# Kernel optimization log

Measured on AMD Instinct MI355X. Metric: run time of the kernel, lower is better.

## Reference

```python
import jax, jax.numpy as jnp
import numpy as np

EPS = 1e-5

def layernorm(x, w, b):
    mu = jnp.mean(x, axis=-1, keepdims=True)
    var = jnp.mean((x - mu) ** 2, axis=-1, keepdims=True)
    return (x - mu) / jnp.sqrt(var + EPS) * w + b

def setup_inputs() -> dict:
    key = jax.random.key(0)
    ks = jax.random.split(key, 20)
    N, E, G = 50000, 800000, 512
    IN, OUT, TXT, MAN = 128, 128, 768, 14
    d = {
        "x": jax.random.normal(ks[0], (N, IN), jnp.float32),
        "edge_index": jax.random.randint(ks[1], (2, E), 0, N),
        "batch": jnp.sort(jax.random.randint(ks[2], (N,), 0, G)),
        "batch_size": G,
        "text_embedding": jax.random.normal(ks[3], (G, TXT), jnp.float32),
        "features_embedding": jax.random.normal(ks[4], (G, MAN), jnp.float32),
        # params
        "ln_proj_w": jnp.ones((IN,)), "ln_proj_b": jnp.zeros((IN,)),
        "W_l": jax.random.normal(ks[5], (IN, OUT)) / np.sqrt(IN),
        "b_l": jnp.zeros((OUT,)),
        "W_r": jax.random.normal(ks[6], (IN, OUT)) / np.sqrt(IN),
        "ln_conv_w": jnp.ones((OUT,)), "ln_conv_b": jnp.zeros((OUT,)),
        "gate_w": jax.random.normal(ks[7], (OUT, 1)) / np.sqrt(OUT),
        "gate_b": jnp.zeros((1,)),
        "graph_weight": jnp.asarray(1.0, jnp.float32),
        "msg_W": jax.random.normal(ks[8], (TXT, OUT)) / np.sqrt(TXT),
        "msg_b": jnp.zeros((OUT,)),
        "feat_W": jax.random.normal(ks[9], (MAN, OUT)) / np.sqrt(MAN),
        "feat_b": jnp.zeros((OUT,)),
        "mixed_w": jnp.ones((3 * OUT,)), "mixed_b": jnp.zeros((3 * OUT,)),
        "fc1_W": jax.random.normal(ks[10], (3 * OUT, 1)) / np.sqrt(3 * OUT),
        "fc1_b": jnp.zeros((1,)),
    }
    return d

def reference(x, edge_index, batch, batch_size, text_embedding, features_embedding,
              ln_proj_w, ln_proj_b, W_l, b_l, W_r, ln_conv_w, ln_conv_b,
              gate_w, gate_b, graph_weight, msg_W, msg_b, feat_W, feat_b,
              mixed_w, mixed_b, fc1_W, fc1_b):
    N = x.shape[0]
    src, dst = edge_index[0], edge_index[1]
    # project_norm
    h = layernorm(x, ln_proj_w, ln_proj_b)
    # GraphSAGE (SAGEConv, mean aggregation): out = mean_j(h_j) @ W_l + b + h @ W_r
    msgs = h[src]                                   # [E, IN] gather
    agg = jax.ops.segment_sum(msgs, dst, num_segments=N)
    deg = jax.ops.segment_sum(jnp.ones((src.shape[0],), h.dtype), dst, num_segments=N)
    mean_nb = agg / jnp.maximum(deg, 1.0)[:, None]
    h = mean_nb @ W_l + b_l + h @ W_r
    # layernorm + gelu (HomogeneousGraphConvolution)
    h = jax.nn.gelu(layernorm(h, ln_conv_w, ln_conv_b), approximate=False)
    # AttentionalAggregation: scatter-softmax over `batch`
    gate = (h @ gate_w + gate_b)[:, 0]              # [N]
    seg_max = jax.ops.segment_max(gate, batch, num_segments=batch_size)
    seg_max = jnp.where(jnp.isfinite(seg_max), seg_max, 0.0)
    e = jnp.exp(gate - seg_max[batch])
    denom = jax.ops.segment_sum(e, batch, num_segments=batch_size)
    attn = (e / denom[batch])[:, None]              # [N,1]
    graph_embedding = jax.ops.segment_sum(attn * h, batch, num_segments=batch_size)
    # dropout is identity in eval mode
    weighted = graph_weight * graph_embedding
    msg_emb = jax.nn.gelu(text_embedding @ msg_W + msg_b, approximate=False)
    feat_emb = jax.nn.gelu(features_embedding @ feat_W + feat_b, approximate=False)
    emb = jnp.concatenate([weighted, msg_emb, feat_emb], axis=1)
    emb = layernorm(emb, mixed_w, mixed_b)
    logits = emb @ fc1_W + fc1_b
    return (logits, graph_embedding, attn)
```

## Files before the change

kernel.cpp:

```cpp
#include <hip/hip_runtime.h>


typedef unsigned short ushort_t;
typedef __attribute__((ext_vector_type(8))) short bf16x8;
typedef __attribute__((ext_vector_type(4))) float floatx4;

#define NBLK 128
#define MAXNB 1024

__device__ __forceinline__ float b2f(ushort_t u) {
    union { unsigned int i; float f; } v; v.i = ((unsigned int)u) << 16; return v.f;
}
__device__ __forceinline__ ushort_t f2b(float f) {
    union { float f; unsigned int i; } v; v.f = f;
    unsigned int x = v.i;
    return (ushort_t)((x + 0x7FFFu + ((x >> 16) & 1u)) >> 16);
}
__device__ __forceinline__ float gelu_f(float x) {
    return 0.5f * x * (1.0f + erff(x * 0.70710678118654752440f));
}
__device__ __forceinline__ float waveReduceSum(float v) {
#pragma unroll
    for (int o = 32; o; o >>= 1) v += __shfl_xor(v, o, 64);
    return v;
}
__device__ __forceinline__ int waveReduceSumI(int v) {
#pragma unroll
    for (int o = 32; o; o >>= 1) v += __shfl_xor(v, o, 64);
    return v;
}
__device__ __forceinline__ float waveReduceMax(float v) {
#pragma unroll
    for (int o = 32; o; o >>= 1) v = fmaxf(v, __shfl_xor(v, o, 64));
    return v;
}
__device__ __forceinline__ int lowerBound(const int* __restrict__ a, int n, int v) {
    int lo = 0, hi = n;
    while (lo < hi) { int mid = (lo + hi) >> 1; if (a[mid] < v) lo = mid + 1; else hi = mid; }
    return lo;
}

__global__ void __launch_bounds__(256) k_prepln(
    const float* __restrict__ x, const float* __restrict__ w, const float* __restrict__ b,
    const float* __restrict__ Wl, const float* __restrict__ Wr,
    ushort_t* __restrict__ Wt, ushort_t* __restrict__ hb, int* __restrict__ deg,
    int* __restrict__ btot, int N, int nb) {
    int bid = blockIdx.x;
    if (bid < 128) {
        if (bid == 0) {
            for (int i = threadIdx.x; i < nb; i += 256) btot[i] = 0;
        }
        int id = bid * 256 + threadIdx.x;
        int n = id >> 8, k = id & 255;
        float v = (k < 128) ? Wl[k * 128 + n] : Wr[(k - 128) * 128 + n];
        Wt[n * 256 + k] = f2b(v);
        return;
    }
    int lb = bid - 128;
    if (threadIdx.x < 4) {
        int rz = lb * 4 + threadIdx.x;
        if (rz < N) deg[rz] = 0;
    }
    int row  = lb * 4 + (threadIdx.x >> 6);
    int lane = threadIdx.x & 63;
    if (row >= N) return;
    size_t base = (size_t)row * 128;
    float2 xv = ((const float2*)(x + base))[lane];
    float v0 = xv.x, v1 = xv.y;
    float s  = waveReduceSum(v0 + v1);
    float s2 = waveReduceSum(v0 * v0 + v1 * v1);
    float mu = s * (1.0f / 128.0f);
    float var = s2 * (1.0f / 128.0f) - mu * mu;
    float rstd = 1.0f / sqrtf(var + 1e-5f);
    int d = lane * 2;
    ushort2 ov;
    ov.x = f2b((v0 - mu) * rstd * w[d]     + b[d]);
    ov.y = f2b((v1 - mu) * rstd * w[d + 1] + b[d + 1]);
    ((ushort2*)(hb + base))[lane] = ov;
}

__global__ void __launch_bounds__(256) k_deghist(
    const int* __restrict__ ei, int* __restrict__ deg, int* __restrict__ bhistT,
    int* __restrict__ btot, int E, int nb, int chunk) {
    __shared__ int hist[MAXNB];
    int blk = blockIdx.x, t = threadIdx.x;
    for (int i = t; i < nb; i += 256) hist[i] = 0;
    __syncthreads();
    int e0 = blk * chunk, e1 = min(e0 + chunk, E);
    for (int e = e0 + t; e < e1; e += 256) {
        int d = ei[E + e];
        atomicAdd(&deg[d], 1);
        atomicAdd(&hist[d >> 7], 1);
    }
    __syncthreads();
    for (int i = t; i < nb; i += 256) {
        int h = hist[i];
        bhistT[(size_t)blk * nb + i] = h;
        if (h) atomicAdd(&btot[i], h);
    }
}

__global__ void __launch_bounds__(256) k_cursor2(
    const int* __restrict__ deg, const int* __restrict__ btot,
    int* __restrict__ cursor, int N) {
    int c = blockIdx.x, t = threadIdx.x;
    __shared__ int sb[256];
    __shared__ int cw[4];
    int lim = c * 2;
    int part = 0;
    for (int bkt = t; bkt < lim; bkt += 256) part += btot[bkt];
    part = waveReduceSumI(part);
    int lane = t & 63, wv = t >> 6;
    if (lane == 0) cw[wv] = part;
    int i = c * 256 + t;
    int v = (i < N) ? deg[i] : 0;
    sb[t] = v;
    __syncthreads();
    for (int o = 1; o < 256; o <<= 1) {
        int a = (t >= o) ? sb[t - o] : 0;
        __syncthreads();
        sb[t] += a;
        __syncthreads();
    }
    int coff = cw[0] + cw[1] + cw[2] + cw[3];
    if (i < N) cursor[i] = sb[t] - v + coff;
}

__global__ void __launch_bounds__(256) k_bplace(
    const int* __restrict__ ei, const int* __restrict__ bhistT,
    const int* __restrict__ cursor, unsigned int* __restrict__ packed,
    int E, int nb, int chunk) {
    __shared__ int lcur[MAXNB];
    int blk = blockIdx.x, t = threadIdx.x;
    int a0 = 0, a1 = 0, a2 = 0, a3 = 0;
    int b0 = t, b1 = t + 256, b2 = t + 512, b3 = t + 768;
    if (b0 < nb) a0 = cursor[b0 << 7];
    if (b1 < nb) a1 = cursor[b1 << 7];
    if (b2 < nb) a2 = cursor[b2 << 7];
    if (b3 < nb) a3 = cursor[b3 << 7];
    for (int c = 0; c < blk; c++) {
        const int* row = bhistT + (size_t)c * nb;
        if (b0 < nb) a0 += row[b0];
        if (b1 < nb) a1 += row[b1];
        if (b2 < nb) a2 += row[b2];
        if (b3 < nb) a3 += row[b3];
    }
    if (b0 < nb) lcur[b0] = a0;
    if (b1 < nb) lcur[b1] = a1;
    if (b2 < nb) lcur[b2] = a2;
    if (b3 < nb) lcur[b3] = a3;
    __syncthreads();
    int e0 = blk * chunk, e1 = min(e0 + chunk, E);
    for (int e = e0 + t; e < e1; e += 256) {
        int s = ei[e], d = ei[E + e];
        int pos = atomicAdd(&lcur[d >> 7], 1);
        packed[pos] = ((unsigned int)(d & 127) << 25) | (unsigned int)s;
    }
}

__global__ void __launch_bounds__(256) k_bsort(
    const unsigned int* __restrict__ packed, const int* __restrict__ cursor,
    int* __restrict__ nbr, int N, int E) {
    __shared__ int lcur[128];
    int b = blockIdx.x, t = threadIdx.x;
    int node0 = b << 7;
    if (t < 128) {
        int node = node0 + t;
        lcur[t] = (node < N) ? cursor[node] : 0;
    }
    __syncthreads();
    int gstart = cursor[node0];
    int next = node0 + 128;
    int gend = (next < N) ? cursor[next] : E;
    for (int i = gstart + t; i < gend; i += 256) {
        unsigned int p = packed[i];
        int pos = atomicAdd(&lcur[p >> 25], 1);
        nbr[pos] = (int)(p & 0x1FFFFFFu);
    }
}

__global__ void __launch_bounds__(256) k_aggemm(
    const ushort_t* __restrict__ hb, const ushort_t* __restrict__ Wt,
    const float* __restrict__ bl, const float* __restrict__ lnw,
    const float* __restrict__ lnb, const float* __restrict__ gw,
    const float* __restrict__ gb, const int* __restrict__ deg,
    const int* __restrict__ cursor, const int* __restrict__ nbr,
    ushort_t* __restrict__ h3b, float* __restrict__ gate, int N) {
    __shared__ ushort_t A[16][264];
    __shared__ float H2[16][132];
    int t = threadIdx.x;
    int row0 = blockIdx.x * 16;
    int w = t >> 6, l = t & 63;
    int sub = l >> 4, li = l & 15;
    for (int rr = 0; rr < 4; rr++) {
        int r = w * 4 + rr;
        int node = row0 + r; if (node >= N) node = N - 1;
        if (sub == 2) {
            bf16x8 hv = *(const bf16x8*)(hb + (size_t)node * 128 + li * 8);
            *(bf16x8*)&A[r][128 + li * 8] = hv;
        }
        int dg = deg[node];
        int st = cursor[node];
        float a0 = 0.f, a1 = 0.f, a2 = 0.f, a3 = 0.f;
        float a4 = 0.f, a5 = 0.f, a6 = 0.f, a7 = 0.f;
        for (int j = 0; j < dg; j += 8) {
            int i0 = j + sub, i1 = j + 4 + sub;
            bf16x8 r0 = {0,0,0,0,0,0,0,0};
            bf16x8 r1 = {0,0,0,0,0,0,0,0};
            if (i0 < dg) {
                int s = nbr[st + i0];
                r0 = *(const bf16x8*)(hb + (size_t)s * 128 + li * 8);
            }
            if (i1 < dg) {
                int s = nbr[st + i1];
                r1 = *(const bf16x8*)(hb + (size_t)s * 128 + li * 8);
            }
            a0 += b2f((ushort_t)r0[0]) + b2f((ushort_t)r1[0]);
            a1 += b2f((ushort_t)r0[1]) + b2f((ushort_t)r1[1]);
            a2 += b2f((ushort_t)r0[2]) + b2f((ushort_t)r1[2]);
            a3 += b2f((ushort_t)r0[3]) + b2f((ushort_t)r1[3]);
            a4 += b2f((ushort_t)r0[4]) + b2f((ushort_t)r1[4]);
            a5 += b2f((ushort_t)r0[5]) + b2f((ushort_t)r1[5]);
            a6 += b2f((ushort_t)r0[6]) + b2f((ushort_t)r1[6]);
            a7 += b2f((ushort_t)r0[7]) + b2f((ushort_t)r1[7]);
        }
        a0 += __shfl_xor(a0, 16, 64); a0 += __shfl_xor(a0, 32, 64);
        a1 += __shfl_xor(a1, 16, 64); a1 += __shfl_xor(a1, 32, 64);
        a2 += __shfl_xor(a2, 16, 64); a2 += __shfl_xor(a2, 32, 64);
        a3 += __shfl_xor(a3, 16, 64); a3 += __shfl_xor(a3, 32, 64);
        a4 += __shfl_xor(a4, 16, 64); a4 += __shfl_xor(a4, 32, 64);
        a5 += __shfl_xor(a5, 16, 64); a5 += __shfl_xor(a5, 32, 64);
        a6 += __shfl_xor(a6, 16, 64); a6 += __shfl_xor(a6, 32, 64);
        a7 += __shfl_xor(a7, 16, 64); a7 += __shfl_xor(a7, 32, 64);
        if (sub == 0) {
            float inv = 1.0f / fmaxf((float)dg, 1.0f);
            bf16x8 ov;
            ov[0] = (short)f2b(a0 * inv); ov[1] = (short)f2b(a1 * inv);
            ov[2] = (short)f2b(a2 * inv); ov[3] = (short)f2b(a3 * inv);
            ov[4] = (short)f2b(a4 * inv); ov[5] = (short)f2b(a5 * inv);
            ov[6] = (short)f2b(a6 * inv); ov[7] = (short)f2b(a7 * inv);
            *(bf16x8*)&A[r][li * 8] = ov;
        }
    }
    __syncthreads();
    int m16 = l & 15, quad = l >> 4;
    int n0 = w * 32 + m16;
    int n1 = n0 + 16;
    floatx4 acc0 = {0.f, 0.f, 0.f, 0.f}, acc1 = {0.f, 0.f, 0.f, 0.f};
    for (int ks = 0; ks < 256; ks += 32) {
        bf16x8 a  = *(const bf16x8*)&A[m16][ks + quad * 8];
        bf16x8 b0 = *(const bf16x8*)(Wt + (size_t)n0 * 256 + ks + quad * 8);
        bf16x8 b1 = *(const bf16x8*)(Wt + (size_t)n1 * 256 + ks + quad * 8);
        acc0 = __builtin_amdgcn_mfma_f32_16x16x32_bf16(a, b0, acc0, 0, 0, 0);
        acc1 = __builtin_amdgcn_mfma_f32_16x16x32_bf16(a, b1, acc1, 0, 0, 0);
    }
#pragma unroll
    for (int i = 0; i < 4; i++) {
        H2[quad * 4 + i][n0] = acc0[i];
        H2[quad * 4 + i][n1] = acc1[i];
    }
    __syncthreads();
    int d = l * 2;
    float bb0 = bl[d],  bb1 = bl[d + 1];
    float lw0 = lnw[d], lw1 = lnw[d + 1];
    float lb0 = lnb[d], lb1 = lnb[d + 1];
    float gw0 = gw[d],  gw1 = gw[d + 1];
    float gbias = gb[0];
#pragma unroll
    for (int rr = 0; rr < 4; rr++) {
        int r = w * 4 + rr;
        int row = row0 + r;
        if (row >= N) break;
        float v0 = H2[r][d] + bb0, v1 = H2[r][d + 1] + bb1;
        float s  = waveReduceSum(v0 + v1);
        float s2 = waveReduceSum(v0 * v0 + v1 * v1);
        float mu = s * (1.f / 128.f);
        float var = s2 * (1.f / 128.f) - mu * mu;
        float rstd = 1.0f / sqrtf(var + 1e-5f);
        float g0 = gelu_f((v0 - mu) * rstd * lw0 + lb0);
        float g1 = gelu_f((v1 - mu) * rstd * lw1 + lb1);
        float gp = waveReduceSum(g0 * gw0 + g1 * gw1);
        ushort2 ov; ov.x = f2b(g0); ov.y = f2b(g1);
        ((ushort2*)(h3b + (size_t)row * 128))[l] = ov;
        if (l == 0) gate[row] = gp + gbias;
    }
}

__global__ void __launch_bounds__(128) k_attntail(
    const float* __restrict__ gate, const ushort_t* __restrict__ h3b,
    const int* __restrict__ batch,
    const float* __restrict__ text, const float* __restrict__ feats,
    const float* __restrict__ msgW, const float* __restrict__ msgb,
    const float* __restrict__ featW, const float* __restrict__ featb,
    const float* __restrict__ gwt, const float* __restrict__ mixw,
    const float* __restrict__ mixb, const float* __restrict__ fc1W,
    const float* __restrict__ fc1b,
    float* __restrict__ ge_out, float* __restrict__ attn_out,
    float* __restrict__ logits, int N, int G) {
    int g = blockIdx.x, t = threadIdx.x;
    __shared__ int sbound[2];
    __shared__ float wbuf[2];
    __shared__ float pbuf[128];
    __shared__ float txt[768];
    __shared__ float rbuf[4];
    if (t < 2) sbound[t] = lowerBound(batch, N, g + t);
    for (int i = t; i < 768; i += 128) txt[i] = text[(size_t)g * 768 + i];
    __syncthreads();
    int s0 = sbound[0], s1 = sbound[1];
    int lane = t & 63, wv = t >> 6;
    float acc = 0.f;
    if (s1 > s0) {
        float m = -3.0e38f;
        for (int i = s0 + t; i < s1; i += 128) m = fmaxf(m, gate[i]);
        m = waveReduceMax(m);
        if (lane == 0) wbuf[wv] = m;
        __syncthreads();
        m = fmaxf(wbuf[0], wbuf[1]);
        __syncthreads();
        float dsum = 0.f;
        for (int i = s0 + t; i < s1; i += 128) dsum += expf(gate[i] - m);
        dsum = waveReduceSum(dsum);
        if (lane == 0) wbuf[wv] = dsum;
        __syncthreads();
        float inv = 1.0f / (wbuf[0] + wbuf[1]);
        for (int base = s0; base < s1; base += 128) {
            int n = min(128, s1 - base);
            __syncthreads();
            if (t < n) {
                float p = expf(gate[base + t] - m) * inv;
                pbuf[t] = p;
                attn_out[base + t] = p;
            }
            __syncthreads();
            for (int j = 0; j < n; j++)
                acc += pbuf[j] * b2f(h3b[(size_t)(base + j) * 128 + t]);
        }
    }
    ge_out[(size_t)g * 128 + t] = acc;
    float am = msgb[t];
    for (int k = 0; k < 768; k += 4) {
        float4 a = *(const float4*)&txt[k];
        am += a.x * msgW[(k + 0) * 128 + t] + a.y * msgW[(k + 1) * 128 + t]
            + a.z * msgW[(k + 2) * 128 + t] + a.w * msgW[(k + 3) * 128 + t];
    }
    float me = gelu_f(am);
    float af = featb[t];
#pragma unroll
    for (int k = 0; k < 14; k++) af += feats[g * 14 + k] * featW[k * 128 + t];
    float fe = gelu_f(af);
    float e0 = gwt[0] * acc;
    float ps = e0 + me + fe, ps2 = e0 * e0 + me * me + fe * fe;
    float r1 = waveReduceSum(ps), r2 = waveReduceSum(ps2);
    __syncthreads();
    if (lane == 0) { rbuf[wv] = r1; rbuf[2 + wv] = r2; }
    __syncthreads();
    float S = rbuf[0] + rbuf[1], S2 = rbuf[2] + rbuf[3];
    float mu = S * (1.f / 384.f);
    float var = S2 * (1.f / 384.f) - mu * mu;
    float rstd = 1.0f / sqrtf(var + 1e-5f);
    float n0 = (e0 - mu) * rstd * mixw[t]       + mixb[t];
    float n1 = (me - mu) * rstd * mixw[128 + t] + mixb[128 + t];
    float n2 = (fe - mu) * rstd * mixw[256 + t] + mixb[256 + t];
    float lp = n0 * fc1W[t] + n1 * fc1W[128 + t] + n2 * fc1W[256 + t];
    float r3 = waveReduceSum(lp);
    __syncthreads();
    if (lane == 0) rbuf[wv] = r3;
    __syncthreads();
    if (t == 0) logits[g] = rbuf[0] + rbuf[1] + fc1b[0];
}

extern "C" void kernel_launch(void* const* d_in, const int* in_sizes, int n_in,
                              void* d_out, int out_size, void* d_ws, size_t ws_size,
                              hipStream_t stream) {
    const float* x     = (const float*)d_in[0];
    const int*   ei    = (const int*)d_in[1];
    const int*   batch = (const int*)d_in[2];
    const float* text  = (const float*)d_in[4];
    const float* feats = (const float*)d_in[5];
    const float* lnpw  = (const float*)d_in[6];
    const float* lnpb  = (const float*)d_in[7];
    const float* Wl    = (const float*)d_in[8];
    const float* bl    = (const float*)d_in[9];
    const float* Wr    = (const float*)d_in[10];
    const float* lncw  = (const float*)d_in[11];
    const float* lncb  = (const float*)d_in[12];
    const float* gatew = (const float*)d_in[13];
    const float* gateb = (const float*)d_in[14];
    const float* gwt   = (const float*)d_in[15];
    const float* msgW  = (const float*)d_in[16];
    const float* msgb  = (const float*)d_in[17];
    const float* featW = (const float*)d_in[18];
    const float* featb = (const float*)d_in[19];
    const float* mixw  = (const float*)d_in[20];
    const float* mixb  = (const float*)d_in[21];
    const float* fc1W  = (const float*)d_in[22];
    const float* fc1b  = (const float*)d_in[23];

    int N = in_sizes[0] / 128;
    int E = in_sizes[1] / 2;
    int G = in_sizes[4] / 768;

    char* wp = (char*)d_ws;
    auto alloc = [&](size_t bytes) -> char* {
        char* p = wp; wp += (bytes + 255) & ~(size_t)255; return p;
    };
    ushort_t* hb     = (ushort_t*)alloc((size_t)N * 128 * 2);
    ushort_t* h3b    = (ushort_t*)alloc((size_t)N * 128 * 2);
    ushort_t* Wt     = (ushort_t*)alloc(128 * 256 * 2);
    float*    gate   = (float*)alloc((size_t)N * 4);
    int*      deg    = (int*)alloc((size_t)N * 4);
    int*      cursor = (int*)alloc((size_t)N * 4);
    int*      nbr    = (int*)alloc((size_t)E * 4);
    unsigned int* packed = (unsigned int*)alloc((size_t)E * 4);

    int nch = (N + 255) / 256;
    int nb  = (N + 127) / 128;
    int chunk = (E + NBLK - 1) / NBLK;

    int* bhistT = (int*)alloc((size_t)NBLK * nb * 4);
    int* btot   = (int*)alloc((size_t)nb * 4);

    float* logits_out = (float*)d_out;
    float* ge_out     = logits_out + G;
    float* attn_out   = ge_out + (size_t)G * 128;

    k_prepln   <<<128 + (N + 3) / 4, 256, 0, stream>>>(x, lnpw, lnpb, Wl, Wr, Wt, hb,
                                                       deg, btot, N, nb);
    k_deghist  <<<NBLK,              256, 0, stream>>>(ei, deg, bhistT, btot, E, nb, chunk);
    k_cursor2  <<<nch,               256, 0, stream>>>(deg, btot, cursor, N);
    k_bplace   <<<NBLK,              256, 0, stream>>>(ei, bhistT, cursor, packed, E, nb, chunk);
    k_bsort    <<<nb,                256, 0, stream>>>(packed, cursor, nbr, N, E);
    k_aggemm   <<<(N + 15) / 16,     256, 0, stream>>>(hb, Wt, bl, lncw, lncb, gatew, gateb,
                                                       deg, cursor, nbr, h3b, gate, N);
    k_attntail <<<G,                 128, 0, stream>>>(gate, h3b, batch, text, feats,
                                                       msgW, msgb, featW, featb, gwt,
                                                       mixw, mixb, fc1W, fc1b,
                                                       ge_out, attn_out, logits_out, N, G);
}
```

Measured before the change: 333.7 us.

## Replace two-pass bucketed CSR build with direct atomic counting scatter

```diff
diff --git a/kernel.cpp b/kernel.cpp
--- a/kernel.cpp
+++ b/kernel.cpp
@@ -4,9 +4,6 @@
 typedef unsigned short ushort_t;
 typedef __attribute__((ext_vector_type(8))) short bf16x8;
 typedef __attribute__((ext_vector_type(4))) float floatx4;
-
-#define NBLK 128
-#define MAXNB 1024
 
 __device__ __forceinline__ float b2f(ushort_t u) {
     union { unsigned int i; float f; } v; v.i = ((unsigned int)u) << 16; return v.f;
@@ -43,13 +40,9 @@
 __global__ void __launch_bounds__(256) k_prepln(
     const float* __restrict__ x, const float* __restrict__ w, const float* __restrict__ b,
     const float* __restrict__ Wl, const float* __restrict__ Wr,
-    ushort_t* __restrict__ Wt, ushort_t* __restrict__ hb, int* __restrict__ deg,
-    int* __restrict__ btot, int N, int nb) {
+    ushort_t* __restrict__ Wt, ushort_t* __restrict__ hb, int* __restrict__ deg, int N) {
     int bid = blockIdx.x;
     if (bid < 128) {
-        if (bid == 0) {
-            for (int i = threadIdx.x; i < nb; i += 256) btot[i] = 0;
-        }
         int id = bid * 256 + threadIdx.x;
         int n = id >> 8, k = id & 255;
         float v = (k < 128) ? Wl[k * 128 + n] : Wr[(k - 128) * 128 + n];
@@ -79,40 +72,34 @@
     ((ushort2*)(hb + base))[lane] = ov;
 }
 
-__global__ void __launch_bounds__(256) k_deghist(
-    const int* __restrict__ ei, int* __restrict__ deg, int* __restrict__ bhistT,
-    int* __restrict__ btot, int E, int nb, int chunk) {
-    __shared__ int hist[MAXNB];
-    int blk = blockIdx.x, t = threadIdx.x;
-    for (int i = t; i < nb; i += 256) hist[i] = 0;
-    __syncthreads();
-    int e0 = blk * chunk, e1 = min(e0 + chunk, E);
-    for (int e = e0 + t; e < e1; e += 256) {
-        int d = ei[E + e];
-        atomicAdd(&deg[d], 1);
-        atomicAdd(&hist[d >> 7], 1);
-    }
-    __syncthreads();
-    for (int i = t; i < nb; i += 256) {
-        int h = hist[i];
-        bhistT[(size_t)blk * nb + i] = h;
-        if (h) atomicAdd(&btot[i], h);
-    }
-}
-
-__global__ void __launch_bounds__(256) k_cursor2(
-    const int* __restrict__ deg, const int* __restrict__ btot,
-    int* __restrict__ cursor, int N) {
+__global__ void __launch_bounds__(256) k_count(
+    const int* __restrict__ ei, int* __restrict__ deg, int E) {
+    int i0 = (blockIdx.x * 256 + threadIdx.x) * 4;
+    const int* dstp = ei + E;
+    if (i0 + 3 < E) {
+        int4 d4 = *(const int4*)(dstp + i0);
+        atomicAdd(&deg[d4.x], 1);
+        atomicAdd(&deg[d4.y], 1);
+        atomicAdd(&deg[d4.z], 1);
+        atomicAdd(&deg[d4.w], 1);
+    } else {
+        int e1 = min(i0 + 4, E);
+        for (int i = i0; i < e1; i++) atomicAdd(&deg[dstp[i]], 1);
+    }
+}
+
+__global__ void __launch_bounds__(256) k_cursor3(
+    const int* __restrict__ deg, int* __restrict__ cursor, int* __restrict__ wcur, int N) {
     int c = blockIdx.x, t = threadIdx.x;
     __shared__ int sb[256];
     __shared__ int cw[4];
-    int lim = c * 2;
+    int lim = c << 8;
     int part = 0;
-    for (int bkt = t; bkt < lim; bkt += 256) part += btot[bkt];
+    for (int j = t; j < lim; j += 256) part += deg[j];
     part = waveReduceSumI(part);
     int lane = t & 63, wv = t >> 6;
     if (lane == 0) cw[wv] = part;
-    int i = c * 256 + t;
+    int i = (c << 8) + t;
     int v = (i < N) ? deg[i] : 0;
     sb[t] = v;
     __syncthreads();
@@ -123,59 +110,29 @@
         __syncthreads();
     }
     int coff = cw[0] + cw[1] + cw[2] + cw[3];
-    if (i < N) cursor[i] = sb[t] - v + coff;
-}
-
-__global__ void __launch_bounds__(256) k_bplace(
-    const int* __restrict__ ei, const int* __restrict__ bhistT,
-    const int* __restrict__ cursor, unsigned int* __restrict__ packed,
-    int E, int nb, int chunk) {
-    __shared__ int lcur[MAXNB];
-    int blk = blockIdx.x, t = threadIdx.x;
-    int a0 = 0, a1 = 0, a2 = 0, a3 = 0;
-    int b0 = t, b1 = t + 256, b2 = t + 512, b3 = t + 768;
-    if (b0 < nb) a0 = cursor[b0 << 7];
-    if (b1 < nb) a1 = cursor[b1 << 7];
-    if (b2 < nb) a2 = cursor[b2 << 7];
-    if (b3 < nb) a3 = cursor[b3 << 7];
-    for (int c = 0; c < blk; c++) {
-        const int* row = bhistT + (size_t)c * nb;
-        if (b0 < nb) a0 += row[b0];
-        if (b1 < nb) a1 += row[b1];
-        if (b2 < nb) a2 += row[b2];
-        if (b3 < nb) a3 += row[b3];
-    }
-    if (b0 < nb) lcur[b0] = a0;
-    if (b1 < nb) lcur[b1] = a1;
-    if (b2 < nb) lcur[b2] = a2;
-    if (b3 < nb) lcur[b3] = a3;
-    __syncthreads();
-    int e0 = blk * chunk, e1 = min(e0 + chunk, E);
-    for (int e = e0 + t; e < e1; e += 256) {
-        int s = ei[e], d = ei[E + e];
-        int pos = atomicAdd(&lcur[d >> 7], 1);
-        packed[pos] = ((unsigned int)(d & 127) << 25) | (unsigned int)s;
-    }
-}
-
-__global__ void __launch_bounds__(256) k_bsort(
-    const unsigned int* __restrict__ packed, const int* __restrict__ cursor,
-    int* __restrict__ nbr, int N, int E) {
-    __shared__ int lcur[128];
-    int b = blockIdx.x, t = threadIdx.x;
-    int node0 = b << 7;
-    if (t < 128) {
-        int node = node0 + t;
-        lcur[t] = (node < N) ? cursor[node] : 0;
-    }
-    __syncthreads();
-    int gstart = cursor[node0];
-    int next = node0 + 128;
-    int gend = (next < N) ? cursor[next] : E;
-    for (int i = gstart + t; i < gend; i += 256) {
-        unsigned int p = packed[i];
-        int pos = atomicAdd(&lcur[p >> 25], 1);
-        nbr[pos] = (int)(p & 0x1FFFFFFu);
+    if (i < N) {
+        int cv = sb[t] - v + coff;
+        cursor[i] = cv;
+        wcur[i]   = cv;
+    }
+}
+
+__global__ void __launch_bounds__(256) k_place(
+    const int* __restrict__ ei, int* __restrict__ wcur, int* __restrict__ nbr, int E) {
+    int i0 = (blockIdx.x * 256 + threadIdx.x) * 4;
+    if (i0 + 3 < E) {
+        int4 s4 = *(const int4*)(ei + i0);
+        int4 d4 = *(const int4*)(ei + E + i0);
+        nbr[atomicAdd(&wcur[d4.x], 1)] = s4.x;
+        nbr[atomicAdd(&wcur[d4.y], 1)] = s4.y;
+        nbr[atomicAdd(&wcur[d4.z], 1)] = s4.z;
+        nbr[atomicAdd(&wcur[d4.w], 1)] = s4.w;
+    } else {
+        int e1 = min(i0 + 4, E);
+        for (int i = i0; i < e1; i++) {
+            int s = ei[i], d = ei[E + i];
+            nbr[atomicAdd(&wcur[d], 1)] = s;
+        }
     }
 }
 
@@ -410,26 +367,20 @@
     float*    gate   = (float*)alloc((size_t)N * 4);
     int*      deg    = (int*)alloc((size_t)N * 4);
     int*      cursor = (int*)alloc((size_t)N * 4);
+    int*      wcur   = (int*)alloc((size_t)N * 4);
     int*      nbr    = (int*)alloc((size_t)E * 4);
-    unsigned int* packed = (unsigned int*)alloc((size_t)E * 4);
 
     int nch = (N + 255) / 256;
-    int nb  = (N + 127) / 128;
-    int chunk = (E + NBLK - 1) / NBLK;
-
-    int* bhistT = (int*)alloc((size_t)NBLK * nb * 4);
-    int* btot   = (int*)alloc((size_t)nb * 4);
+    int eb  = (E + 1023) / 1024;
 
     float* logits_out = (float*)d_out;
     float* ge_out     = logits_out + G;
     float* attn_out   = ge_out + (size_t)G * 128;
 
-    k_prepln   <<<128 + (N + 3) / 4, 256, 0, stream>>>(x, lnpw, lnpb, Wl, Wr, Wt, hb,
-                                                       deg, btot, N, nb);
-    k_deghist  <<<NBLK,              256, 0, stream>>>(ei, deg, bhistT, btot, E, nb, chunk);
-    k_cursor2  <<<nch,               256, 0, stream>>>(deg, btot, cursor, N);
-    k_bplace   <<<NBLK,              256, 0, stream>>>(ei, bhistT, cursor, packed, E, nb, chunk);
-    k_bsort    <<<nb,                256, 0, stream>>>(packed, cursor, nbr, N, E);
+    k_prepln   <<<128 + (N + 3) / 4, 256, 0, stream>>>(x, lnpw, lnpb, Wl, Wr, Wt, hb, deg, N);
+    k_count    <<<eb,                256, 0, stream>>>(ei, deg, E);
+    k_cursor3  <<<nch,               256, 0, stream>>>(deg, cursor, wcur, N);
+    k_place    <<<eb,                256, 0, stream>>>(ei, wcur, nbr, E);
     k_aggemm   <<<(N + 15) / 16,     256, 0, stream>>>(hb, Wt, bl, lncw, lncb, gatew, gateb,
                                                        deg, cursor, nbr, h3b, gate, N);
     k_attntail <<<G,                 128, 0, stream>>>(gate, h3b, batch, text, feats,
```

Result: faster. 325.7 us (-2.4%).
